# Performance work log

Hardware: AMD Instinct MI355X
Metric: run time of the kernel (lower is better)

Reference implementation:

```python
import jax, jax.numpy as jnp
import numpy as np

N = 50000
E = 800000
IN_DIM = 512
H1 = IN_DIM // 2   # 256
H2 = IN_DIM // 4   # 128
D = 8
NP_CAYLEY = D * (D - 1) // 2  # 28


def setup_inputs() -> dict:
    key = jax.random.key(0)
    ks = jax.random.split(key, 10)
    x = jax.random.normal(ks[0], (N, IN_DIM), dtype=jnp.float32)
    edge_index = jax.random.randint(ks[1], (2, E), 0, N, dtype=jnp.int64)
    s1 = 1.0 / np.sqrt(IN_DIM)
    s2 = 1.0 / np.sqrt(H1)
    s3 = 1.0 / np.sqrt(H2)
    W1l = jax.random.uniform(ks[2], (H1, IN_DIM), jnp.float32, -s1, s1)
    b1 = jax.random.uniform(ks[3], (H1,), jnp.float32, -s1, s1)
    W1r = jax.random.uniform(ks[4], (H1, IN_DIM), jnp.float32, -s1, s1)
    W2l = jax.random.uniform(ks[5], (H2, H1), jnp.float32, -s2, s2)
    b2 = jax.random.uniform(ks[6], (H2,), jnp.float32, -s2, s2)
    W2r = jax.random.uniform(ks[7], (H2, H1), jnp.float32, -s2, s2)
    Wp = jax.random.uniform(ks[8], (NP_CAYLEY, H2), jnp.float32, -s3, s3)
    bp = jax.random.uniform(ks[9], (NP_CAYLEY,), jnp.float32, -s3, s3)
    return {"x": x, "edge_index": edge_index,
            "W1l": W1l, "b1": b1, "W1r": W1r,
            "W2l": W2l, "b2": b2, "W2r": W2r,
            "Wp": Wp, "bp": bp}


def _sage_conv(x, src, dst, Wl, bl, Wr):
    # PyG SAGEConv (mean aggr): out = lin_l(mean_{j in N(i)} x_j) + lin_r(x_i)
    msg_sum = jax.ops.segment_sum(x[src], dst, num_segments=N)  # [N, F]
    deg = jax.ops.segment_sum(jnp.ones((src.shape[0],), x.dtype), dst,
                              num_segments=N)
    mean = msg_sum / jnp.maximum(deg, 1.0)[:, None]
    return mean @ Wl.T + bl + x @ Wr.T


def _cayley(params):
    # params: [N, d(d-1)/2] -> skew A, then O = (I - A)^{-1} (I + A)
    iu, ju = jnp.triu_indices(D, k=1)  # row-major i<j matches torch loop order
    n = params.shape[0]
    A = jnp.zeros((n, D, D), params.dtype)
    A = A.at[:, iu, ju].set(params)
    A = A.at[:, ju, iu].set(-params)
    I = jnp.eye(D, dtype=params.dtype)
    return jnp.linalg.solve(I[None] - A, I[None] + A)


def reference(x, edge_index, W1l, b1, W1r, W2l, b2, W2r, Wp, bp):
    src, dst = edge_index[0], edge_index[1]
    h = jax.nn.relu(_sage_conv(x, src, dst, W1l, b1, W1r))
    h = jax.nn.relu(_sage_conv(h, src, dst, W2l, b2, W2r))
    params = h @ Wp.T + bp  # [N, 28]
    return _cayley(params)  # [N, 8, 8]
```

## Files before the change

kernel.cpp:

```cpp
#include <hip/hip_runtime.h>
#include <hip/hip_bf16.h>


#define WS_ALIGN(x) (((x) + 255) & ~size_t(255))

typedef __attribute__((ext_vector_type(8))) short short8;
typedef __attribute__((ext_vector_type(4))) float floatx4;

static __device__ __forceinline__ ushort f2b(float f) {
    unsigned u = __builtin_bit_cast(unsigned, f);
    u = (u + 0x7fffu + ((u >> 16) & 1u)) >> 16;
    return (ushort)u;
}
static __device__ __forceinline__ float b2f(ushort h) {
    unsigned u = ((unsigned)h) << 16;
    return __builtin_bit_cast(float, u);
}


__global__ void hist_kernel(const int* __restrict__ dst, int* __restrict__ deg, int E) {
    int e = blockIdx.x * blockDim.x + threadIdx.x;
    if (e < E) atomicAdd(&deg[dst[e]], 1);
}

__global__ __launch_bounds__(256)
void scan_phase1(const int* __restrict__ deg, int* __restrict__ bsum, int n) {
    __shared__ int red[256];
    const int t = threadIdx.x;
    const int i = blockIdx.x * 1024 + t * 4;
    int s = 0;
    if (i + 4 <= n) {
        int4 v = *reinterpret_cast<const int4*>(&deg[i]);
        s = v.x + v.y + v.z + v.w;
    } else {
        for (int k = i; k < n; ++k) s += deg[k];
    }
    red[t] = s;
    __syncthreads();
#pragma unroll
    for (int off = 128; off > 0; off >>= 1) {
        if (t < off) red[t] += red[t + off];
        __syncthreads();
    }
    if (t == 0) bsum[blockIdx.x] = red[0];
}

__global__ __launch_bounds__(256)
void scan_phase2(int* __restrict__ bsum, int* __restrict__ rowptr, int nb, int n) {
    __shared__ int sh[256];
    const int t = threadIdx.x;
    int orig = (t < nb) ? bsum[t] : 0;
    sh[t] = orig;
    __syncthreads();
#pragma unroll
    for (int off = 1; off < 256; off <<= 1) {
        int v = (t >= off) ? sh[t - off] : 0;
        __syncthreads();
        sh[t] += v;
        __syncthreads();
    }
    if (t < nb) bsum[t] = sh[t] - orig;
    if (t == 255) rowptr[n] = sh[255];
}

__global__ __launch_bounds__(256)
void scan_phase3(const int* __restrict__ deg, const int* __restrict__ bsum,
                 int* __restrict__ rowptr, int n) {
    __shared__ int red[256];
    const int t = threadIdx.x;
    const int i = blockIdx.x * 1024 + t * 4;
    int v0 = 0, v1 = 0, v2 = 0, v3 = 0;
    if (i + 4 <= n) {
        int4 v = *reinterpret_cast<const int4*>(&deg[i]);
        v0 = v.x; v1 = v.y; v2 = v.z; v3 = v.w;
    } else {
        if (i     < n) v0 = deg[i];
        if (i + 1 < n) v1 = deg[i + 1];
        if (i + 2 < n) v2 = deg[i + 2];
        if (i + 3 < n) v3 = deg[i + 3];
    }
    int s = v0 + v1 + v2 + v3;
    red[t] = s;
    __syncthreads();
#pragma unroll
    for (int off = 1; off < 256; off <<= 1) {
        int u = (t >= off) ? red[t - off] : 0;
        __syncthreads();
        red[t] += u;
        __syncthreads();
    }
    int pre = bsum[blockIdx.x] + red[t] - s;
    if (i + 4 <= n) {
        int4 o;
        o.x = pre; o.y = pre + v0; o.z = pre + v0 + v1; o.w = pre + v0 + v1 + v2;
        *reinterpret_cast<int4*>(&rowptr[i]) = o;
    } else {
        if (i     < n) rowptr[i]     = pre;
        if (i + 1 < n) rowptr[i + 1] = pre + v0;
        if (i + 2 < n) rowptr[i + 2] = pre + v0 + v1;
        if (i + 3 < n) rowptr[i + 3] = pre + v0 + v1 + v2;
    }
}

__global__ void scatter_kernel(const int* __restrict__ src, const int* __restrict__ dst,
                               const int* __restrict__ rowptr, int* __restrict__ cursor,
                               int* __restrict__ adj, int E) {
    int e = blockIdx.x * blockDim.x + threadIdx.x;
    if (e < E) {
        int d = dst[e];
        int p = atomicAdd(&cursor[d], 1);
        adj[rowptr[d] + p] = src[e];
    }
}


__global__ void cast_kernel(const float* __restrict__ src, ushort* __restrict__ dst, int n8) {
    for (int i = blockIdx.x * blockDim.x + threadIdx.x; i < n8; i += gridDim.x * blockDim.x) {
        const float4* s4 = reinterpret_cast<const float4*>(src + (size_t)i * 8);
        float4 v0 = s4[0], v1 = s4[1];
        short8 o;
        o[0] = (short)f2b(v0.x); o[1] = (short)f2b(v0.y);
        o[2] = (short)f2b(v0.z); o[3] = (short)f2b(v0.w);
        o[4] = (short)f2b(v1.x); o[5] = (short)f2b(v1.y);
        o[6] = (short)f2b(v1.z); o[7] = (short)f2b(v1.w);
        *reinterpret_cast<short8*>(dst + (size_t)i * 8) = o;
    }
}

__global__ void build_wcat(const float* __restrict__ W1l, const float* __restrict__ W1r,
                           const float* __restrict__ W2l, const float* __restrict__ W2r,
                           ushort* __restrict__ Wc1, ushort* __restrict__ Wc2) {
    int idx = blockIdx.x * blockDim.x + threadIdx.x;
    const int n1 = (512 * 512) / 8;
    const int n2 = (256 * 256) / 8;
    const float* src;
    ushort* dst;
    if (idx < n1) {
        int e = idx * 8;
        int row = e >> 9, col = e & 511;
        src = (row < 256) ? &W1l[row * 512 + col] : &W1r[(row - 256) * 512 + col];
        dst = &Wc1[e];
    } else if (idx < n1 + n2) {
        int e = (idx - n1) * 8;
        int row = e >> 8, col = e & 255;
        src = (row < 128) ? &W2l[row * 256 + col] : &W2r[(row - 128) * 256 + col];
        dst = &Wc2[e];
    } else {
        return;
    }
    const float4* s4 = reinterpret_cast<const float4*>(src);
    float4 v0 = s4[0], v1 = s4[1];
    short8 o;
    o[0] = (short)f2b(v0.x); o[1] = (short)f2b(v0.y);
    o[2] = (short)f2b(v0.z); o[3] = (short)f2b(v0.w);
    o[4] = (short)f2b(v1.x); o[5] = (short)f2b(v1.y);
    o[6] = (short)f2b(v1.z); o[7] = (short)f2b(v1.w);
    *reinterpret_cast<short8*>(dst) = o;
}


__global__ __launch_bounds__(256)
void gemm_bf16(const ushort* __restrict__ A, const ushort* __restrict__ B,
               ushort* __restrict__ Cl, ushort* __restrict__ Cr,
               int M, int K, int Ncols, int S) {
    __shared__ ushort As[128 * 64];
    __shared__ ushort Bs[128 * 64];
    const int tid  = threadIdx.x;
    const int wave = tid >> 6;
    const int lane = tid & 63;
    const int row0 = blockIdx.y * 128;
    const int col0 = blockIdx.x * 128;
    const int wm = (wave & 1) * 64;
    const int wn = (wave >> 1) * 64;

    floatx4 acc[4][4];
#pragma unroll
    for (int i = 0; i < 4; ++i)
#pragma unroll
        for (int j = 0; j < 4; ++j)
            acc[i][j] = (floatx4){0.f, 0.f, 0.f, 0.f};

    const int rsub = lane >> 3;
    const int ksw  = ((lane & 7) * 16) ^ (rsub << 4);

    for (int k0 = 0; k0 < K; k0 += 64) {
#pragma unroll
        for (int i = 0; i < 4; ++i) {
            int chunk = wave * 4 + i;
            int r = chunk * 8 + rsub;
            int grow = row0 + r;
            if (grow >= M) grow = M - 1;
            const char* src = (const char*)(A + (size_t)grow * K + k0) + ksw;
            __builtin_amdgcn_global_load_lds(
                (const __attribute__((address_space(1))) unsigned int*)src,
                (__attribute__((address_space(3))) unsigned int*)(&As[chunk * 512]),
                16, 0, 0);
        }
#pragma unroll
        for (int i = 0; i < 4; ++i) {
            int chunk = wave * 4 + i;
            int r = chunk * 8 + rsub;
            int gcol = col0 + r;
            const char* src = (const char*)(B + (size_t)gcol * K + k0) + ksw;
            __builtin_amdgcn_global_load_lds(
                (const __attribute__((address_space(1))) unsigned int*)src,
                (__attribute__((address_space(3))) unsigned int*)(&Bs[chunk * 512]),
                16, 0, 0);
        }
        __syncthreads();

#pragma unroll
        for (int kk = 0; kk < 2; ++kk) {
            short8 af[4], bf[4];
            const int kb = (kk * 64 + ((lane >> 4) << 4)) ^ ((lane & 7) << 4);
#pragma unroll
            for (int im = 0; im < 4; ++im) {
                int r = wm + im * 16 + (lane & 15);
                af[im] = *reinterpret_cast<const short8*>((const char*)As + r * 128 + kb);
            }
#pragma unroll
            for (int in = 0; in < 4; ++in) {
                int r = wn + in * 16 + (lane & 15);
                bf[in] = *reinterpret_cast<const short8*>((const char*)Bs + r * 128 + kb);
            }
#pragma unroll
            for (int im = 0; im < 4; ++im)
#pragma unroll
                for (int in = 0; in < 4; ++in)
                    acc[im][in] = __builtin_amdgcn_mfma_f32_16x16x32_bf16(
                        af[im], bf[in], acc[im][in], 0, 0, 0);
        }
        __syncthreads();
    }

    ushort* Cbase = (col0 < S) ? Cl : Cr;
    const int cb = (col0 < S) ? col0 : col0 - S;
#pragma unroll
    for (int im = 0; im < 4; ++im) {
#pragma unroll
        for (int reg = 0; reg < 4; ++reg) {
            int r = row0 + wm + im * 16 + ((lane >> 4) << 2) + reg;
            if (r < M) {
                size_t base = (size_t)r * S + cb + wn + (lane & 15);
#pragma unroll
                for (int in = 0; in < 4; ++in)
                    Cbase[base + in * 16] = f2b(acc[im][in][reg]);
            }
        }
    }
}


template <int LPN>
__global__ __launch_bounds__(256)
void aggregate_bf16(const ushort* __restrict__ Yl, const ushort* __restrict__ Yr,
                    const float* __restrict__ bias,
                    const int* __restrict__ rowptr, const int* __restrict__ adj,
                    ushort* __restrict__ H, int n) {
    constexpr int F = LPN * 4;
    const int grp = threadIdx.x / LPN;
    const int sub = threadIdx.x % LPN;
    const int node = blockIdx.x * (256 / LPN) + grp;
    if (node >= n) return;
    const int c = sub * 4;
    const int start = rowptr[node], end = rowptr[node + 1];

    float a0 = 0.f, a1 = 0.f, a2 = 0.f, a3 = 0.f;
    int e = start;
    for (; e + 4 <= end; e += 4) {
        int s0 = adj[e + 0], s1 = adj[e + 1], s2 = adj[e + 2], s3 = adj[e + 3];
        ushort4 r0 = *reinterpret_cast<const ushort4*>(&Yl[(size_t)s0 * F + c]);
        ushort4 r1 = *reinterpret_cast<const ushort4*>(&Yl[(size_t)s1 * F + c]);
        ushort4 r2 = *reinterpret_cast<const ushort4*>(&Yl[(size_t)s2 * F + c]);
        ushort4 r3 = *reinterpret_cast<const ushort4*>(&Yl[(size_t)s3 * F + c]);
        a0 += (b2f(r0.x) + b2f(r1.x)) + (b2f(r2.x) + b2f(r3.x));
        a1 += (b2f(r0.y) + b2f(r1.y)) + (b2f(r2.y) + b2f(r3.y));
        a2 += (b2f(r0.z) + b2f(r1.z)) + (b2f(r2.z) + b2f(r3.z));
        a3 += (b2f(r0.w) + b2f(r1.w)) + (b2f(r2.w) + b2f(r3.w));
    }
    for (; e < end; ++e) {
        int s = adj[e];
        ushort4 r = *reinterpret_cast<const ushort4*>(&Yl[(size_t)s * F + c]);
        a0 += b2f(r.x); a1 += b2f(r.y); a2 += b2f(r.z); a3 += b2f(r.w);
    }

    const int d = end - start;
    const float inv = 1.0f / (float)(d > 0 ? d : 1);
    ushort4 sv = *reinterpret_cast<const ushort4*>(&Yr[(size_t)node * F + c]);
    float4 bv = *reinterpret_cast<const float4*>(&bias[c]);
    ushort4 o;
    o.x = f2b(fmaxf(a0 * inv + b2f(sv.x) + bv.x, 0.f));
    o.y = f2b(fmaxf(a1 * inv + b2f(sv.y) + bv.y, 0.f));
    o.z = f2b(fmaxf(a2 * inv + b2f(sv.z) + bv.z, 0.f));
    o.w = f2b(fmaxf(a3 * inv + b2f(sv.w) + bv.w, 0.f));
    *reinterpret_cast<ushort4*>(&H[(size_t)node * F + c]) = o;
}


__global__ __launch_bounds__(256)
void params_kernel(const ushort* __restrict__ H2, const float* __restrict__ Wp,
                   const float* __restrict__ bp, float* __restrict__ P, int n) {
    __shared__ float WpS[32 * 132];
    __shared__ float bpS[32];
    for (int t = threadIdx.x; t < 32 * 132; t += 256) WpS[t] = 0.f;
    if (threadIdx.x < 32) bpS[threadIdx.x] = (threadIdx.x < 28) ? bp[threadIdx.x] : 0.f;
    __syncthreads();
    for (int t = threadIdx.x; t < 28 * 128; t += 256) {
        int r = t >> 7, c = t & 127;
        WpS[r * 132 + c] = Wp[t];
    }
    __syncthreads();

    const int node = blockIdx.x * 32 + (threadIdx.x >> 3);
    const int l = threadIdx.x & 7;
    if (node >= n) return;

    short8 h8[16];
    const short8* hp = reinterpret_cast<const short8*>(&H2[(size_t)node * 128]);
#pragma unroll
    for (int q = 0; q < 16; ++q) h8[q] = hp[q];

    float acc0 = bpS[l], acc1 = bpS[l + 8], acc2 = bpS[l + 16], acc3 = bpS[l + 24];
#pragma unroll
    for (int q = 0; q < 32; ++q) {
        float h0 = b2f((ushort)h8[q >> 1][(q & 1) * 4 + 0]);
        float h1 = b2f((ushort)h8[q >> 1][(q & 1) * 4 + 1]);
        float h2 = b2f((ushort)h8[q >> 1][(q & 1) * 4 + 2]);
        float h3 = b2f((ushort)h8[q >> 1][(q & 1) * 4 + 3]);
        float4 w0 = *reinterpret_cast<const float4*>(&WpS[(l +  0) * 132 + 4 * q]);
        float4 w1 = *reinterpret_cast<const float4*>(&WpS[(l +  8) * 132 + 4 * q]);
        float4 w2 = *reinterpret_cast<const float4*>(&WpS[(l + 16) * 132 + 4 * q]);
        float4 w3 = *reinterpret_cast<const float4*>(&WpS[(l + 24) * 132 + 4 * q]);
        acc0 += h0 * w0.x + h1 * w0.y + h2 * w0.z + h3 * w0.w;
        acc1 += h0 * w1.x + h1 * w1.y + h2 * w1.z + h3 * w1.w;
        acc2 += h0 * w2.x + h1 * w2.y + h2 * w2.z + h3 * w2.w;
        acc3 += h0 * w3.x + h1 * w3.y + h2 * w3.z + h3 * w3.w;
    }
    float* pout = &P[(size_t)node * 32];
    pout[l]      = acc0;
    pout[l + 8]  = acc1;
    pout[l + 16] = acc2;
    pout[l + 24] = acc3;
}


__global__ __launch_bounds__(256)
void cayley_kernel(const float* __restrict__ P, float* __restrict__ Out, int n) {
    int i = blockIdx.x * blockDim.x + threadIdx.x;
    if (i >= n) return;
    float p[28];
    const float4* pp = reinterpret_cast<const float4*>(&P[(size_t)i * 32]);
#pragma unroll
    for (int q = 0; q < 7; ++q) {
        float4 v = pp[q];
        p[4 * q + 0] = v.x; p[4 * q + 1] = v.y;
        p[4 * q + 2] = v.z; p[4 * q + 3] = v.w;
    }

    float M_[8][8], B_[8][8];
#pragma unroll
    for (int r = 0; r < 8; ++r)
#pragma unroll
        for (int c = 0; c < 8; ++c) {
            M_[r][c] = (r == c) ? 1.f : 0.f;
            B_[r][c] = (r == c) ? 1.f : 0.f;
        }
    {
        int idx = 0;
#pragma unroll
        for (int r = 0; r < 8; ++r)
#pragma unroll
            for (int c = r + 1; c < 8; ++c) {
                float a = p[idx++];
                M_[r][c] -= a;  M_[c][r] += a;
                B_[r][c] += a;  B_[c][r] -= a;
            }
    }
#pragma unroll
    for (int col = 0; col < 8; ++col) {
        float inv = 1.0f / M_[col][col];
#pragma unroll
        for (int c = 0; c < 8; ++c) { M_[col][c] *= inv; B_[col][c] *= inv; }
#pragma unroll
        for (int r = 0; r < 8; ++r) {
            if (r == col) continue;
            float f = M_[r][col];
#pragma unroll
            for (int c = 0; c < 8; ++c) {
                M_[r][c] -= f * M_[col][c];
                B_[r][c] -= f * B_[col][c];
            }
        }
    }
    float* out = &Out[(size_t)i * 64];
#pragma unroll
    for (int r = 0; r < 8; ++r) {
        float4 o0 = make_float4(B_[r][0], B_[r][1], B_[r][2], B_[r][3]);
        float4 o1 = make_float4(B_[r][4], B_[r][5], B_[r][6], B_[r][7]);
        *reinterpret_cast<float4*>(&out[r * 8 + 0]) = o0;
        *reinterpret_cast<float4*>(&out[r * 8 + 4]) = o1;
    }
}


extern "C" void kernel_launch(void* const* d_in, const int* in_sizes, int n_in,
                              void* d_out, int out_size, void* d_ws, size_t ws_size,
                              hipStream_t stream) {
    const float* x   = (const float*)d_in[0];
    const int*   ei  = (const int*)d_in[1];
    const float* W1l = (const float*)d_in[2];
    const float* b1  = (const float*)d_in[3];
    const float* W1r = (const float*)d_in[4];
    const float* W2l = (const float*)d_in[5];
    const float* b2  = (const float*)d_in[6];
    const float* W2r = (const float*)d_in[7];
    const float* Wp  = (const float*)d_in[8];
    const float* bp  = (const float*)d_in[9];
    float* out = (float*)d_out;

    const int IN_DIM = 512;
    const int N = in_sizes[0] / IN_DIM;
    const int E = in_sizes[1] / 2;

    char* ws = (char*)d_ws;
    size_t off = 0;
    int* deg      = (int*)(ws + off); off = WS_ALIGN(off + (size_t)N * 4);
    int* rowptr   = (int*)(ws + off); off = WS_ALIGN(off + (size_t)(N + 1) * 4);
    int* cursor   = (int*)(ws + off); off = WS_ALIGN(off + (size_t)N * 4);
    int* bsum     = (int*)(ws + off); off = WS_ALIGN(off + (size_t)256 * 4);
    int* adj      = (int*)(ws + off); off = WS_ALIGN(off + (size_t)E * 4);
    ushort* xb    = (ushort*)(ws + off); off = WS_ALIGN(off + (size_t)N * 512 * 2);
    ushort* Yl    = (ushort*)(ws + off); off = WS_ALIGN(off + (size_t)N * 256 * 2);
    ushort* Yr    = (ushort*)(ws + off); off = WS_ALIGN(off + (size_t)N * 256 * 2);
    ushort* h1    = (ushort*)(ws + off); off = WS_ALIGN(off + (size_t)N * 256 * 2);
    ushort* Wc1   = (ushort*)(ws + off); off = WS_ALIGN(off + (size_t)512 * 512 * 2);
    ushort* Wc2   = (ushort*)(ws + off); off = WS_ALIGN(off + (size_t)256 * 256 * 2);
    float*  Pp    = (float*)(ws + off);  off = WS_ALIGN(off + (size_t)N * 32 * 4);

    const int* src = ei;
    const int* dst = ei + E;

    hipMemsetAsync(deg, 0, (size_t)N * 4, stream);
    hipMemsetAsync(cursor, 0, (size_t)N * 4, stream);

    int eb = (E + 255) / 256;
    int nb = (N + 1023) / 1024;
    hist_kernel<<<eb, 256, 0, stream>>>(dst, deg, E);
    scan_phase1<<<nb, 256, 0, stream>>>(deg, bsum, N);
    scan_phase2<<<1, 256, 0, stream>>>(bsum, rowptr, nb, N);
    scan_phase3<<<nb, 256, 0, stream>>>(deg, bsum, rowptr, N);
    scatter_kernel<<<eb, 256, 0, stream>>>(src, dst, rowptr, cursor, adj, E);

    cast_kernel<<<1024, 256, 0, stream>>>(x, xb, N * 512 / 8);
    build_wcat<<<((512 * 512 + 256 * 256) / 8 + 255) / 256, 256, 0, stream>>>(
        W1l, W1r, W2l, W2r, Wc1, Wc2);

    int gm = (N + 127) / 128;

    gemm_bf16<<<dim3(4, gm), 256, 0, stream>>>(xb, Wc1, Yl, Yr, N, 512, 512, 256);
    aggregate_bf16<64><<<(N + 3) / 4, 256, 0, stream>>>(Yl, Yr, b1, rowptr, adj, h1, N);

    ushort* zl = xb;
    ushort* zr = xb + (size_t)N * 128;
    gemm_bf16<<<dim3(2, gm), 256, 0, stream>>>(h1, Wc2, zl, zr, N, 256, 256, 128);
    ushort* h2 = Yl;
    aggregate_bf16<32><<<(N + 7) / 8, 256, 0, stream>>>(zl, zr, b2, rowptr, adj, h2, N);

    params_kernel<<<(N + 31) / 32, 256, 0, stream>>>(h2, Wp, bp, Pp, N);
    cayley_kernel<<<(N + 255) / 256, 256, 0, stream>>>(Pp, out, N);
}
```

Before: 301.5 us.

## Fuse fp32-to-bf16 cast into GEMM, widen GEMM tiles, vectorize aggregation

The standalone cast kernel for x goes away. The first GEMM now reads fp32 rows, converts them to bf16 in registers and writes them into swizzled LDS. Both GEMMs move to 128x256 tiles, so each block covers more output columns and the A operand is re-read fewer times, at the cost of more accumulator registers and a two-block-per-CU launch bound. The aggregation kernels now load 8 bf16 values per lane instead of 4, which halves the number of lanes per node. The fused cast gives up the asynchronous global-to-LDS path for A in the first GEMM.

```diff
diff --git a/kernel.cpp b/kernel.cpp
--- a/kernel.cpp
+++ b/kernel.cpp
@@ -15,6 +15,9 @@
 static __device__ __forceinline__ float b2f(ushort h) {
     unsigned u = ((unsigned)h) << 16;
     return __builtin_bit_cast(float, u);
+}
+static __device__ __forceinline__ unsigned pk2(float a, float b) {
+    return (unsigned)f2b(a) | ((unsigned)f2b(b) << 16);
 }
 
 
@@ -110,20 +113,6 @@
         int d = dst[e];
         int p = atomicAdd(&cursor[d], 1);
         adj[rowptr[d] + p] = src[e];
-    }
-}
-
-
-__global__ void cast_kernel(const float* __restrict__ src, ushort* __restrict__ dst, int n8) {
-    for (int i = blockIdx.x * blockDim.x + threadIdx.x; i < n8; i += gridDim.x * blockDim.x) {
-        const float4* s4 = reinterpret_cast<const float4*>(src + (size_t)i * 8);
-        float4 v0 = s4[0], v1 = s4[1];
-        short8 o;
-        o[0] = (short)f2b(v0.x); o[1] = (short)f2b(v0.y);
-        o[2] = (short)f2b(v0.z); o[3] = (short)f2b(v0.w);
-        o[4] = (short)f2b(v1.x); o[5] = (short)f2b(v1.y);
-        o[6] = (short)f2b(v1.z); o[7] = (short)f2b(v1.w);
-        *reinterpret_cast<short8*>(dst + (size_t)i * 8) = o;
     }
 }
 
@@ -159,46 +148,70 @@
 }
 
 
-__global__ __launch_bounds__(256)
-void gemm_bf16(const ushort* __restrict__ A, const ushort* __restrict__ B,
+template <bool CASTA>
+__global__ __launch_bounds__(256, 2)
+void gemm_wide(const float* __restrict__ Af, const ushort* __restrict__ Ab,
+               const ushort* __restrict__ B,
                ushort* __restrict__ Cl, ushort* __restrict__ Cr,
                int M, int K, int Ncols, int S) {
     __shared__ ushort As[128 * 64];
-    __shared__ ushort Bs[128 * 64];
+    __shared__ ushort Bs[256 * 64];
     const int tid  = threadIdx.x;
     const int wave = tid >> 6;
     const int lane = tid & 63;
     const int row0 = blockIdx.y * 128;
-    const int col0 = blockIdx.x * 128;
+    const int col0 = blockIdx.x * 256;
     const int wm = (wave & 1) * 64;
-    const int wn = (wave >> 1) * 64;
-
-    floatx4 acc[4][4];
+    const int wn = (wave >> 1) * 128;
+
+    floatx4 acc[4][8];
 #pragma unroll
     for (int i = 0; i < 4; ++i)
 #pragma unroll
-        for (int j = 0; j < 4; ++j)
+        for (int j = 0; j < 8; ++j)
             acc[i][j] = (floatx4){0.f, 0.f, 0.f, 0.f};
 
     const int rsub = lane >> 3;
     const int ksw  = ((lane & 7) * 16) ^ (rsub << 4);
 
     for (int k0 = 0; k0 < K; k0 += 64) {
-#pragma unroll
-        for (int i = 0; i < 4; ++i) {
-            int chunk = wave * 4 + i;
-            int r = chunk * 8 + rsub;
-            int grow = row0 + r;
-            if (grow >= M) grow = M - 1;
-            const char* src = (const char*)(A + (size_t)grow * K + k0) + ksw;
-            __builtin_amdgcn_global_load_lds(
-                (const __attribute__((address_space(1))) unsigned int*)src,
-                (__attribute__((address_space(3))) unsigned int*)(&As[chunk * 512]),
-                16, 0, 0);
-        }
-#pragma unroll
-        for (int i = 0; i < 4; ++i) {
-            int chunk = wave * 4 + i;
+        if constexpr (CASTA) {
+            const int r = tid >> 1, h = tid & 1;
+            int grow = row0 + r; if (grow >= M) grow = M - 1;
+            const float* srow = Af + (size_t)grow * K + k0 + h * 32;
+            char* lrow = (char*)As + r * 128;
+            const int rx = (r & 7) << 4;
+#pragma unroll
+            for (int half = 0; half < 2; ++half) {
+                float4 v0 = *reinterpret_cast<const float4*>(srow + half * 16 + 0);
+                float4 v1 = *reinterpret_cast<const float4*>(srow + half * 16 + 4);
+                float4 v2 = *reinterpret_cast<const float4*>(srow + half * 16 + 8);
+                float4 v3 = *reinterpret_cast<const float4*>(srow + half * 16 + 12);
+                int g0 = h * 4 + half * 2;
+                uint4 o0 = make_uint4(pk2(v0.x, v0.y), pk2(v0.z, v0.w),
+                                      pk2(v1.x, v1.y), pk2(v1.z, v1.w));
+                uint4 o1 = make_uint4(pk2(v2.x, v2.y), pk2(v2.z, v2.w),
+                                      pk2(v3.x, v3.y), pk2(v3.z, v3.w));
+                *reinterpret_cast<uint4*>(lrow + ((g0 * 16) ^ rx))       = o0;
+                *reinterpret_cast<uint4*>(lrow + (((g0 + 1) * 16) ^ rx)) = o1;
+            }
+        } else {
+#pragma unroll
+            for (int i = 0; i < 4; ++i) {
+                int chunk = wave * 4 + i;
+                int r = chunk * 8 + rsub;
+                int grow = row0 + r;
+                if (grow >= M) grow = M - 1;
+                const char* src = (const char*)(Ab + (size_t)grow * K + k0) + ksw;
+                __builtin_amdgcn_global_load_lds(
+                    (const __attribute__((address_space(1))) unsigned int*)src,
+                    (__attribute__((address_space(3))) unsigned int*)(&As[chunk * 512]),
+                    16, 0, 0);
+            }
+        }
+#pragma unroll
+        for (int i = 0; i < 8; ++i) {
+            int chunk = wave * 8 + i;
             int r = chunk * 8 + rsub;
             int gcol = col0 + r;
             const char* src = (const char*)(B + (size_t)gcol * K + k0) + ksw;
@@ -211,7 +224,7 @@
 
 #pragma unroll
         for (int kk = 0; kk < 2; ++kk) {
-            short8 af[4], bf[4];
+            short8 af[4], bf[8];
             const int kb = (kk * 64 + ((lane >> 4) << 4)) ^ ((lane & 7) << 4);
 #pragma unroll
             for (int im = 0; im < 4; ++im) {
@@ -219,32 +232,32 @@
                 af[im] = *reinterpret_cast<const short8*>((const char*)As + r * 128 + kb);
             }
 #pragma unroll
-            for (int in = 0; in < 4; ++in) {
+            for (int in = 0; in < 8; ++in) {
                 int r = wn + in * 16 + (lane & 15);
                 bf[in] = *reinterpret_cast<const short8*>((const char*)Bs + r * 128 + kb);
             }
 #pragma unroll
             for (int im = 0; im < 4; ++im)
 #pragma unroll
-                for (int in = 0; in < 4; ++in)
+                for (int in = 0; in < 8; ++in)
                     acc[im][in] = __builtin_amdgcn_mfma_f32_16x16x32_bf16(
                         af[im], bf[in], acc[im][in], 0, 0, 0);
         }
         __syncthreads();
     }
 
-    ushort* Cbase = (col0 < S) ? Cl : Cr;
-    const int cb = (col0 < S) ? col0 : col0 - S;
 #pragma unroll
     for (int im = 0; im < 4; ++im) {
 #pragma unroll
         for (int reg = 0; reg < 4; ++reg) {
             int r = row0 + wm + im * 16 + ((lane >> 4) << 2) + reg;
             if (r < M) {
-                size_t base = (size_t)r * S + cb + wn + (lane & 15);
-#pragma unroll
-                for (int in = 0; in < 4; ++in)
-                    Cbase[base + in * 16] = f2b(acc[im][in][reg]);
+#pragma unroll
+                for (int in = 0; in < 8; ++in) {
+                    int g = col0 + wn + in * 16 + (lane & 15);
+                    if (g < S) Cl[(size_t)r * S + g] = f2b(acc[im][in][reg]);
+                    else       Cr[(size_t)r * S + (g - S)] = f2b(acc[im][in][reg]);
+                }
             }
         }
     }
@@ -257,43 +270,48 @@
                     const float* __restrict__ bias,
                     const int* __restrict__ rowptr, const int* __restrict__ adj,
                     ushort* __restrict__ H, int n) {
-    constexpr int F = LPN * 4;
+    constexpr int F = LPN * 8;
     const int grp = threadIdx.x / LPN;
     const int sub = threadIdx.x % LPN;
     const int node = blockIdx.x * (256 / LPN) + grp;
     if (node >= n) return;
-    const int c = sub * 4;
+    const int c = sub * 8;
     const int start = rowptr[node], end = rowptr[node + 1];
 
-    float a0 = 0.f, a1 = 0.f, a2 = 0.f, a3 = 0.f;
+    float acc[8];
+#pragma unroll
+    for (int v = 0; v < 8; ++v) acc[v] = 0.f;
+
     int e = start;
     for (; e + 4 <= end; e += 4) {
         int s0 = adj[e + 0], s1 = adj[e + 1], s2 = adj[e + 2], s3 = adj[e + 3];
-        ushort4 r0 = *reinterpret_cast<const ushort4*>(&Yl[(size_t)s0 * F + c]);
-        ushort4 r1 = *reinterpret_cast<const ushort4*>(&Yl[(size_t)s1 * F + c]);
-        ushort4 r2 = *reinterpret_cast<const ushort4*>(&Yl[(size_t)s2 * F + c]);
-        ushort4 r3 = *reinterpret_cast<const ushort4*>(&Yl[(size_t)s3 * F + c]);
-        a0 += (b2f(r0.x) + b2f(r1.x)) + (b2f(r2.x) + b2f(r3.x));
-        a1 += (b2f(r0.y) + b2f(r1.y)) + (b2f(r2.y) + b2f(r3.y));
-        a2 += (b2f(r0.z) + b2f(r1.z)) + (b2f(r2.z) + b2f(r3.z));
-        a3 += (b2f(r0.w) + b2f(r1.w)) + (b2f(r2.w) + b2f(r3.w));
+        short8 r0 = *reinterpret_cast<const short8*>(&Yl[(size_t)s0 * F + c]);
+        short8 r1 = *reinterpret_cast<const short8*>(&Yl[(size_t)s1 * F + c]);
+        short8 r2 = *reinterpret_cast<const short8*>(&Yl[(size_t)s2 * F + c]);
+        short8 r3 = *reinterpret_cast<const short8*>(&Yl[(size_t)s3 * F + c]);
+#pragma unroll
+        for (int v = 0; v < 8; ++v)
+            acc[v] += (b2f((ushort)r0[v]) + b2f((ushort)r1[v])) +
+                      (b2f((ushort)r2[v]) + b2f((ushort)r3[v]));
     }
     for (; e < end; ++e) {
         int s = adj[e];
-        ushort4 r = *reinterpret_cast<const ushort4*>(&Yl[(size_t)s * F + c]);
-        a0 += b2f(r.x); a1 += b2f(r.y); a2 += b2f(r.z); a3 += b2f(r.w);
+        short8 r = *reinterpret_cast<const short8*>(&Yl[(size_t)s * F + c]);
+#pragma unroll
+        for (int v = 0; v < 8; ++v) acc[v] += b2f((ushort)r[v]);
     }
 
     const int d = end - start;
     const float inv = 1.0f / (float)(d > 0 ? d : 1);
-    ushort4 sv = *reinterpret_cast<const ushort4*>(&Yr[(size_t)node * F + c]);
-    float4 bv = *reinterpret_cast<const float4*>(&bias[c]);
-    ushort4 o;
-    o.x = f2b(fmaxf(a0 * inv + b2f(sv.x) + bv.x, 0.f));
-    o.y = f2b(fmaxf(a1 * inv + b2f(sv.y) + bv.y, 0.f));
-    o.z = f2b(fmaxf(a2 * inv + b2f(sv.z) + bv.z, 0.f));
-    o.w = f2b(fmaxf(a3 * inv + b2f(sv.w) + bv.w, 0.f));
-    *reinterpret_cast<ushort4*>(&H[(size_t)node * F + c]) = o;
+    short8 sv = *reinterpret_cast<const short8*>(&Yr[(size_t)node * F + c]);
+    float4 bv0 = *reinterpret_cast<const float4*>(&bias[c]);
+    float4 bv1 = *reinterpret_cast<const float4*>(&bias[c + 4]);
+    float bb[8] = {bv0.x, bv0.y, bv0.z, bv0.w, bv1.x, bv1.y, bv1.z, bv1.w};
+    short8 o;
+#pragma unroll
+    for (int v = 0; v < 8; ++v)
+        o[v] = (short)f2b(fmaxf(acc[v] * inv + b2f((ushort)sv[v]) + bb[v], 0.f));
+    *reinterpret_cast<short8*>(&H[(size_t)node * F + c]) = o;
 }
 
 
@@ -429,10 +447,11 @@
     int* cursor   = (int*)(ws + off); off = WS_ALIGN(off + (size_t)N * 4);
     int* bsum     = (int*)(ws + off); off = WS_ALIGN(off + (size_t)256 * 4);
     int* adj      = (int*)(ws + off); off = WS_ALIGN(off + (size_t)E * 4);
-    ushort* xb    = (ushort*)(ws + off); off = WS_ALIGN(off + (size_t)N * 512 * 2);
     ushort* Yl    = (ushort*)(ws + off); off = WS_ALIGN(off + (size_t)N * 256 * 2);
     ushort* Yr    = (ushort*)(ws + off); off = WS_ALIGN(off + (size_t)N * 256 * 2);
     ushort* h1    = (ushort*)(ws + off); off = WS_ALIGN(off + (size_t)N * 256 * 2);
+    ushort* zl    = (ushort*)(ws + off); off = WS_ALIGN(off + (size_t)N * 128 * 2);
+    ushort* zr    = (ushort*)(ws + off); off = WS_ALIGN(off + (size_t)N * 128 * 2);
     ushort* Wc1   = (ushort*)(ws + off); off = WS_ALIGN(off + (size_t)512 * 512 * 2);
     ushort* Wc2   = (ushort*)(ws + off); off = WS_ALIGN(off + (size_t)256 * 256 * 2);
     float*  Pp    = (float*)(ws + off);  off = WS_ALIGN(off + (size_t)N * 32 * 4);
@@ -451,20 +470,19 @@
     scan_phase3<<<nb, 256, 0, stream>>>(deg, bsum, rowptr, N);
     scatter_kernel<<<eb, 256, 0, stream>>>(src, dst, rowptr, cursor, adj, E);
 
-    cast_kernel<<<1024, 256, 0, stream>>>(x, xb, N * 512 / 8);
     build_wcat<<<((512 * 512 + 256 * 256) / 8 + 255) / 256, 256, 0, stream>>>(
         W1l, W1r, W2l, W2r, Wc1, Wc2);
 
     int gm = (N + 127) / 128;
 
-    gemm_bf16<<<dim3(4, gm), 256, 0, stream>>>(xb, Wc1, Yl, Yr, N, 512, 512, 256);
-    aggregate_bf16<64><<<(N + 3) / 4, 256, 0, stream>>>(Yl, Yr, b1, rowptr, adj, h1, N);
-
-    ushort* zl = xb;
-    ushort* zr = xb + (size_t)N * 128;
-    gemm_bf16<<<dim3(2, gm), 256, 0, stream>>>(h1, Wc2, zl, zr, N, 256, 256, 128);
+    gemm_wide<true><<<dim3(2, gm), 256, 0, stream>>>(
+        x, (const ushort*)nullptr, Wc1, Yl, Yr, N, 512, 512, 256);
+    aggregate_bf16<32><<<(N + 7) / 8, 256, 0, stream>>>(Yl, Yr, b1, rowptr, adj, h1, N);
+
+    gemm_wide<false><<<dim3(1, gm), 256, 0, stream>>>(
+        (const float*)nullptr, h1, Wc2, zl, zr, N, 256, 256, 128);
     ushort* h2 = Yl;
-    aggregate_bf16<32><<<(N + 7) / 8, 256, 0, stream>>>(zl, zr, b2, rowptr, adj, h2, N);
+    aggregate_bf16<16><<<(N + 15) / 16, 256, 0, stream>>>(zl, zr, b2, rowptr, adj, h2, N);
 
     params_kernel<<<(N + 31) / 32, 256, 0, stream>>>(h2, Wp, bp, Pp, N);
     cayley_kernel<<<(N + 255) / 256, 256, 0, stream>>>(Pp, out, N);
```

Measured after the change: 295.4 us. 1.02x faster.
